# Kernel tuning notes

Hardware: AMD Instinct MI355X
Metric: run time of the kernel (lower is better)

## Reference

```python
import jax, jax.numpy as jnp
import numpy as np

T, N, E = 8, 5000, 160000
IN_DIM, HID, H = 64, 128, 8
D = HID // H  # head dim = 16
NC = 2
EPS = 1e-5


def layer_norm(x, g, b):
    mu = jnp.mean(x, axis=-1, keepdims=True)
    var = jnp.mean((x - mu) ** 2, axis=-1, keepdims=True)
    return (x - mu) / jnp.sqrt(var + EPS) * g + b


def setup_inputs() -> dict:
    key = jax.random.key(0)
    ks = jax.random.split(key, 24)
    p = {}
    p["x"] = jax.random.normal(ks[0], (T, N, IN_DIM), dtype=jnp.float32)
    p["edge_index"] = jax.random.randint(ks[1], (T, 2, E), 0, N, dtype=jnp.int32)
    p["noise"] = jax.random.normal(ks[2], (N, HID), dtype=jnp.float32)
    def w(k, shape, fan_in):
        return jax.random.normal(k, shape, dtype=jnp.float32) * (1.0 / np.sqrt(fan_in))
    p["W_proj"] = w(ks[3], (IN_DIM, HID), IN_DIM)
    p["b_proj"] = jnp.zeros((HID,), jnp.float32)
    p["W_gat"] = w(ks[4], (HID, HID), HID)
    p["a_src"] = w(ks[5], (H, D), D)
    p["a_dst"] = w(ks[6], (H, D), D)
    p["b_gat"] = jnp.zeros((HID,), jnp.float32)
    p["g1"] = jnp.ones((HID,), jnp.float32)
    p["be1"] = jnp.zeros((HID,), jnp.float32)
    p["W_qkv"] = w(ks[7], (3 * HID, HID), HID)
    p["b_qkv"] = jnp.zeros((3 * HID,), jnp.float32)
    p["W_o"] = w(ks[8], (HID, HID), HID)
    p["b_o"] = jnp.zeros((HID,), jnp.float32)
    p["g2"] = jnp.ones((HID,), jnp.float32)
    p["be2"] = jnp.zeros((HID,), jnp.float32)
    p["Wc1"] = w(ks[9], (HID, HID), HID)
    p["bc1"] = jnp.zeros((HID,), jnp.float32)
    p["gc"] = jnp.ones((HID,), jnp.float32)
    p["bec"] = jnp.zeros((HID,), jnp.float32)
    p["Wc2"] = w(ks[10], (HID, NC), HID)
    p["bc2"] = jnp.array([0.0, 0.1], jnp.float32)
    return p


def reference(x, edge_index, noise, W_proj, b_proj, W_gat, a_src, a_dst, b_gat,
              g1, be1, W_qkv, b_qkv, W_o, b_o, g2, be2,
              Wc1, bc1, gc, bec, Wc2, bc2):
    # per-timestep projection + ReLU: [T, N, HID]
    h = jax.nn.relu(x @ W_proj + b_proj)

    loop = jnp.arange(N, dtype=edge_index.dtype)

    def gat(h_t, ei):  # h_t: [N, HID], ei: [2, E]
        src = jnp.concatenate([ei[0], loop])  # add self loops
        dst = jnp.concatenate([ei[1], loop])
        xh = (h_t @ W_gat).reshape(N, H, D)          # [N, H, D]
        a_s = jnp.sum(xh * a_src, axis=-1)           # [N, H]
        a_d = jnp.sum(xh * a_dst, axis=-1)           # [N, H]
        e = jax.nn.leaky_relu(a_s[src] + a_d[dst], 0.2)  # [E', H]
        m = jax.ops.segment_max(e, dst, num_segments=N)
        ex = jnp.exp(e - m[dst])
        s = jax.ops.segment_sum(ex, dst, num_segments=N)
        alpha = ex / (s[dst] + 1e-16)                # segment softmax per dst/head
        out = jax.ops.segment_sum(xh[src] * alpha[..., None], dst, num_segments=N)
        return out.reshape(N, HID) + b_gat

    feats = jax.vmap(gat)(h, edge_index)             # [T, N, HID]
    nf = jnp.transpose(feats, (1, 0, 2))             # [N, T, HID] (node = batch)

    nrm = layer_norm(nf, g1, be1)
    qkv = nrm @ W_qkv.T + b_qkv                      # [N, T, 3*HID]
    q, k, v = jnp.split(qkv, 3, axis=-1)
    def heads(t):
        return t.reshape(N, T, H, D).transpose(0, 2, 1, 3)  # [N, H, T, D]
    q, k, v = heads(q), heads(k), heads(v)
    scores = jnp.einsum('nhqd,nhkd->nhqk', q, k) / jnp.sqrt(jnp.float32(D))
    attn = jax.nn.softmax(scores, axis=-1)
    ta = jnp.einsum('nhqk,nhkd->nhqd', attn, v)
    ta = ta.transpose(0, 2, 1, 3).reshape(N, T, HID) @ W_o.T + b_o

    fused = layer_norm(nf + ta, g2, be2)
    emb = fused[:, -1, :]                            # [N, HID]

    node_ids = jnp.arange(N, dtype=jnp.float32) / N
    div = jnp.sin(node_ids * 6.28) * 0.1             # [N]
    emb = emb + div[:, None] + noise * 0.05          # eval noise scale

    h1 = emb @ Wc1 + bc1
    h1 = jax.nn.gelu(layer_norm(h1, gc, bec), approximate=False)
    logits = h1 @ Wc2 + bc2                          # [N, 2]
    sinu = jnp.sin(jnp.arange(N, dtype=jnp.float32) * 0.5) * 0.2
    logits = logits.at[:, 1].add(sinu)
    return emb, logits
```

## Files before the change

### kernel.cpp

```cpp
#include <hip/hip_runtime.h>
#include <math.h>

#define T 8
#define N 5000
#define E 160000
#define EN (E + N)
#define IN_DIM 64
#define HID 128
#define H 8
#define D 16
#define NC 2
#define MT 32
#define NB 4

__device__ __forceinline__ float leaky(float e) { return (e >= 0.0f) ? e : 0.2f * e; }

__global__ __launch_bounds__(256) void k_pg(const float* __restrict__ x,
                                            const float* __restrict__ Wp,
                                            const float* __restrict__ bp,
                                            const float* __restrict__ Wg,
                                            const float* __restrict__ asrc,
                                            const float* __restrict__ adst,
                                            float* __restrict__ xh,
                                            float* __restrict__ a_s,
                                            float* __restrict__ a_d,
                                            int* __restrict__ cursor) {
    __shared__ float xt[MT][IN_DIM];
    __shared__ float ht[MT][HID + 1];
    int row0 = blockIdx.x * MT;
    int tid = threadIdx.x;

    {
        int gi = blockIdx.x * 256 + tid;
        if (gi < T * N) cursor[gi] = 0;
    }

    for (int idx = tid; idx < MT * IN_DIM; idx += 256) {
        int r = idx >> 6, k = idx & 63;
        xt[r][k] = x[(size_t)(row0 + r) * IN_DIM + k];
    }
    __syncthreads();

    int cg = tid & 31;
    int rg = tid >> 5;
    int c0 = cg * 4, r0 = rg * 4;

    {
        float4 b4 = *(const float4*)(bp + c0);
        float a00=b4.x,a01=b4.y,a02=b4.z,a03=b4.w;
        float a10=b4.x,a11=b4.y,a12=b4.z,a13=b4.w;
        float a20=b4.x,a21=b4.y,a22=b4.z,a23=b4.w;
        float a30=b4.x,a31=b4.y,a32=b4.z,a33=b4.w;
        for (int k = 0; k < IN_DIM; ++k) {
            float4 w = *(const float4*)(Wp + (size_t)k * HID + c0);
            float x0 = xt[r0 + 0][k], x1 = xt[r0 + 1][k];
            float x2 = xt[r0 + 2][k], x3 = xt[r0 + 3][k];
            a00 += x0*w.x; a01 += x0*w.y; a02 += x0*w.z; a03 += x0*w.w;
            a10 += x1*w.x; a11 += x1*w.y; a12 += x1*w.z; a13 += x1*w.w;
            a20 += x2*w.x; a21 += x2*w.y; a22 += x2*w.z; a23 += x2*w.w;
            a30 += x3*w.x; a31 += x3*w.y; a32 += x3*w.z; a33 += x3*w.w;
        }
        ht[r0+0][c0+0]=fmaxf(a00,0.f); ht[r0+0][c0+1]=fmaxf(a01,0.f);
        ht[r0+0][c0+2]=fmaxf(a02,0.f); ht[r0+0][c0+3]=fmaxf(a03,0.f);
        ht[r0+1][c0+0]=fmaxf(a10,0.f); ht[r0+1][c0+1]=fmaxf(a11,0.f);
        ht[r0+1][c0+2]=fmaxf(a12,0.f); ht[r0+1][c0+3]=fmaxf(a13,0.f);
        ht[r0+2][c0+0]=fmaxf(a20,0.f); ht[r0+2][c0+1]=fmaxf(a21,0.f);
        ht[r0+2][c0+2]=fmaxf(a22,0.f); ht[r0+2][c0+3]=fmaxf(a23,0.f);
        ht[r0+3][c0+0]=fmaxf(a30,0.f); ht[r0+3][c0+1]=fmaxf(a31,0.f);
        ht[r0+3][c0+2]=fmaxf(a32,0.f); ht[r0+3][c0+3]=fmaxf(a33,0.f);
    }
    __syncthreads();

    float a00=0,a01=0,a02=0,a03=0, a10=0,a11=0,a12=0,a13=0;
    float a20=0,a21=0,a22=0,a23=0, a30=0,a31=0,a32=0,a33=0;
    for (int k = 0; k < HID; ++k) {
        float4 w = *(const float4*)(Wg + (size_t)k * HID + c0);
        float h0 = ht[r0 + 0][k], h1 = ht[r0 + 1][k];
        float h2 = ht[r0 + 2][k], h3 = ht[r0 + 3][k];
        a00 += h0*w.x; a01 += h0*w.y; a02 += h0*w.z; a03 += h0*w.w;
        a10 += h1*w.x; a11 += h1*w.y; a12 += h1*w.z; a13 += h1*w.w;
        a20 += h2*w.x; a21 += h2*w.y; a22 += h2*w.z; a23 += h2*w.w;
        a30 += h3*w.x; a31 += h3*w.y; a32 += h3*w.z; a33 += h3*w.w;
    }
    {
        float4 v;
        v.x=a00; v.y=a01; v.z=a02; v.w=a03;
        *(float4*)(xh + (size_t)(row0 + r0 + 0) * HID + c0) = v;
        v.x=a10; v.y=a11; v.z=a12; v.w=a13;
        *(float4*)(xh + (size_t)(row0 + r0 + 1) * HID + c0) = v;
        v.x=a20; v.y=a21; v.z=a22; v.w=a23;
        *(float4*)(xh + (size_t)(row0 + r0 + 2) * HID + c0) = v;
        v.x=a30; v.y=a31; v.z=a32; v.w=a33;
        *(float4*)(xh + (size_t)(row0 + r0 + 3) * HID + c0) = v;
    }
    __syncthreads();
    ht[r0+0][c0+0]=a00; ht[r0+0][c0+1]=a01; ht[r0+0][c0+2]=a02; ht[r0+0][c0+3]=a03;
    ht[r0+1][c0+0]=a10; ht[r0+1][c0+1]=a11; ht[r0+1][c0+2]=a12; ht[r0+1][c0+3]=a13;
    ht[r0+2][c0+0]=a20; ht[r0+2][c0+1]=a21; ht[r0+2][c0+2]=a22; ht[r0+2][c0+3]=a23;
    ht[r0+3][c0+0]=a30; ht[r0+3][c0+1]=a31; ht[r0+3][c0+2]=a32; ht[r0+3][c0+3]=a33;
    __syncthreads();

    {
        int r = tid >> 3, hh = tid & 7;
        float s1 = 0.0f, s2 = 0.0f;
        #pragma unroll
        for (int d = 0; d < D; ++d) {
            float v = ht[r][hh * D + d];
            s1 += v * asrc[hh * D + d];
            s2 += v * adst[hh * D + d];
        }
        a_s[(size_t)(row0 + r) * H + hh] = s1;
        a_d[(size_t)(row0 + r) * H + hh] = s2;
    }
}

__global__ void k_tr(const float* __restrict__ W_qkv, const float* __restrict__ W_o,
                     float* __restrict__ WTq, float* __restrict__ WoT) {
    int idx = blockIdx.x * 256 + threadIdx.x;
    if (idx < 384 * 128) {
        int j = idx >> 7, c = idx & 127;
        WTq[c * 384 + j] = W_qkv[idx];
    } else if (idx < 384 * 128 + 128 * 128) {
        int r = idx - 384 * 128;
        int j = r >> 7, k = r & 127;
        WoT[k * 128 + j] = W_o[r];
    }
}

__global__ __launch_bounds__(256) void k_hist(const int* __restrict__ ei,
                                              int* __restrict__ cursor) {
    __shared__ int hist[N];
    int t = blockIdx.x >> 3;
    int chunk = blockIdx.x & 7;
    int tid = threadIdx.x;

    for (int i = tid; i < N; i += 256) hist[i] = 0;
    __syncthreads();

    const int CS = (EN + 7) / 8;
    int i0 = chunk * CS;
    int i1 = (i0 + CS < EN) ? i0 + CS : EN;
    const int* drow = ei + (size_t)(2 * t + 1) * E;
    for (int i = i0 + tid; i < i1; i += 256) {
        int d = (i < E) ? drow[i] : (i - E);
        atomicAdd(&hist[d], 1);
    }
    __syncthreads();

    int* cur = cursor + t * N;
    for (int i = tid; i < N; i += 256) {
        int c = hist[i];
        if (c) atomicAdd(&cur[i], c);
    }
}

__global__ void k_scan(int* __restrict__ cursor, int* __restrict__ offs) {
    __shared__ int part[256];
    int t = blockIdx.x;
    int tid = threadIdx.x;
    const int CH = 20;
    int begin = tid * CH;
    int sum = 0;
    for (int k = 0; k < CH; ++k) {
        int i = begin + k;
        if (i < N) sum += cursor[t * N + i];
    }
    part[tid] = sum;
    __syncthreads();
    if (tid == 0) {
        int run = 0;
        for (int i = 0; i < 256; ++i) { int v = part[i]; part[i] = run; run += v; }
        offs[t * (N + 1) + N] = run;
    }
    __syncthreads();
    int run = part[tid];
    for (int k = 0; k < CH; ++k) {
        int i = begin + k;
        if (i < N) {
            int cnt = cursor[t * N + i];
            offs[t * (N + 1) + i] = run;
            cursor[t * N + i] = run;
            run += cnt;
        }
    }
}

__global__ __launch_bounds__(256) void k_scatter(const int* __restrict__ ei,
                                                 int* __restrict__ cursor,
                                                 int* __restrict__ csr_src) {
    const int PT = EN / 4;
    int idx = blockIdx.x * 256 + threadIdx.x;
    int t = idx / PT;
    if (t >= T) return;
    int e0 = idx - t * PT;

    const int* srow = ei + (size_t)(2 * t) * E;
    const int* drow = srow + E;
    int s[4], d[4];
    #pragma unroll
    for (int j = 0; j < 4; ++j) {
        int i = e0 + j * PT;
        if (i < E) { s[j] = srow[i]; d[j] = drow[i]; }
        else       { s[j] = d[j] = i - E; }
    }
    int* cur = cursor + t * N;
    int p[4];
    #pragma unroll
    for (int j = 0; j < 4; ++j) p[j] = atomicAdd(&cur[d[j]], 1);
    int* csb = csr_src + (size_t)t * EN;
    #pragma unroll
    for (int j = 0; j < 4; ++j) csb[p[j]] = s[j];
}

__global__ __launch_bounds__(128) void k_aggc(
        const int* __restrict__ offs, const int* __restrict__ csr_src,
        const float* __restrict__ a_s, const float* __restrict__ a_d,
        const float* __restrict__ xh, const float* __restrict__ b_gat,
        const float* __restrict__ g1, const float* __restrict__ be1,
        float* __restrict__ nrm, float* __restrict__ xlast_g) {
    int b = blockIdx.x;
    int t = b & 7;
    int dst = b >> 3;
    int tid = threadIdx.x;

    int o0 = offs[t * (N + 1) + dst];
    int o1 = offs[t * (N + 1) + dst + 1];
    int deg = o1 - o0;
    const int* esrc = csr_src + (size_t)t * EN + o0;
    const float* as_b = a_s + (size_t)t * N * H;
    const float* ad_b = a_d + (size_t)t * N * H;
    const float* xh_b = xh + (size_t)t * N * HID;

    __shared__ float lal[16][H];
    __shared__ int   lsrc[16];
    __shared__ float ws_s[2][H];
    __shared__ float pacc[2][HID];
    __shared__ float red[128];

    int eh_e = tid >> 3, eh_h = tid & 7;
    int el = tid >> 5, cg = tid & 31;
    int hg = cg >> 2;
    float adh_e = ad_b[dst * H + eh_h];

    float4 acc = {0.0f, 0.0f, 0.0f, 0.0f};
    float wpart = 0.0f;

    int ntile = (deg + 15) >> 4;
    for (int tt = 0; tt < ntile; ++tt) {
        int ej = (tt << 4) + eh_e;
        float w = 0.0f;
        int src = 0;
        if (ej < deg) {
            src = esrc[ej];
            w = expf(leaky(as_b[src * H + eh_h] + adh_e));
        }
        if (eh_h == 0) lsrc[eh_e] = src;
        lal[eh_e][eh_h] = w;
        wpart += w;
        __syncthreads();
        #pragma unroll
        for (int jj = 0; jj < 4; ++jj) {
            int j = (jj << 2) + el;
            int s = lsrc[j];
            float l = lal[j][hg];
            float4 v = *(const float4*)(xh_b + (size_t)s * HID + (cg << 2));
            acc.x += l * v.x; acc.y += l * v.y;
            acc.z += l * v.z; acc.w += l * v.w;
        }
        __syncthreads();
    }

    {
        float w = wpart;
        w += __shfl_xor(w, 8);
        w += __shfl_xor(w, 16);
        w += __shfl_xor(w, 32);
        if ((tid & 63) < 8) ws_s[tid >> 6][eh_h] = w;
    }
    acc.x += __shfl_xor(acc.x, 32);
    acc.y += __shfl_xor(acc.y, 32);
    acc.z += __shfl_xor(acc.z, 32);
    acc.w += __shfl_xor(acc.w, 32);
    if (!(tid & 32)) *(float4*)&pacc[tid >> 6][(tid & 31) << 2] = acc;
    __syncthreads();

    int hh = tid >> 4;
    float wsum = ws_s[0][hh] + ws_s[1][hh];
    float val = (pacc[0][tid] + pacc[1][tid]) / (wsum + 1e-16f);

    float v = val + b_gat[tid];
    red[tid] = v;
    __syncthreads();
    if (tid < 64) {
        float s = red[tid] + red[tid + 64];
        #pragma unroll
        for (int m = 1; m < 64; m <<= 1) s += __shfl_xor(s, m);
        if (tid == 0) red[0] = s;
    }
    __syncthreads();
    float mu = red[0] * (1.0f / HID);
    __syncthreads();
    float dv = v - mu;
    red[tid] = dv * dv;
    __syncthreads();
    if (tid < 64) {
        float s = red[tid] + red[tid + 64];
        #pragma unroll
        for (int m = 1; m < 64; m <<= 1) s += __shfl_xor(s, m);
        if (tid == 0) red[0] = s;
    }
    __syncthreads();
    float rstd = rsqrtf(red[0] * (1.0f / HID) + 1e-5f);

    nrm[(size_t)(dst * T + t) * HID + tid] = dv * rstd * g1[tid] + be1[tid];
    if (t == T - 1) xlast_g[(size_t)dst * HID + tid] = v;
}

__global__ __launch_bounds__(256) void k_fuse(
        const float* __restrict__ nrm,
        const float* __restrict__ WTq,
        const float* __restrict__ b_qkv,
        const float* __restrict__ xlast_g,
        const float* __restrict__ WoT,
        const float* __restrict__ b_o,
        const float* __restrict__ g2, const float* __restrict__ be2,
        const float* __restrict__ noise, float* __restrict__ out) {
    __shared__ float at[NB * T][HID];
    __shared__ float kvl[2][NB * T][HID + 2];
    __shared__ float ql[NB][HID];
    float* attn_s = &at[0][0];
    float* ta_s   = &at[0][0] + 256;

    int n0 = blockIdx.x * NB;
    int tid = threadIdx.x;

    {
        const float* src = nrm + (size_t)n0 * T * HID;
        for (int idx = tid; idx < NB * T * 32; idx += 256) {
            int r = idx >> 5, c4 = (idx & 31) << 2;
            *(float4*)&at[r][c4] = *(const float4*)(src + (size_t)r * HID + c4);
        }
    }
    __syncthreads();

    int cg = tid & 31, rg = tid >> 5;
    int c0 = cg * 4, r0 = rg * 4;

    #pragma unroll
    for (int g = 0; g < 2; ++g) {
        int co = 128 + g * 128 + c0;
        float4 b4 = *(const float4*)(b_qkv + co);
        float a00=b4.x,a01=b4.y,a02=b4.z,a03=b4.w;
        float a10=b4.x,a11=b4.y,a12=b4.z,a13=b4.w;
        float a20=b4.x,a21=b4.y,a22=b4.z,a23=b4.w;
        float a30=b4.x,a31=b4.y,a32=b4.z,a33=b4.w;
        for (int k = 0; k < HID; ++k) {
            float4 w = *(const float4*)(WTq + (size_t)k * 384 + co);
            float e0 = at[r0+0][k], e1 = at[r0+1][k];
            float e2 = at[r0+2][k], e3 = at[r0+3][k];
            a00 += e0*w.x; a01 += e0*w.y; a02 += e0*w.z; a03 += e0*w.w;
            a10 += e1*w.x; a11 += e1*w.y; a12 += e1*w.z; a13 += e1*w.w;
            a20 += e2*w.x; a21 += e2*w.y; a22 += e2*w.z; a23 += e2*w.w;
            a30 += e3*w.x; a31 += e3*w.y; a32 += e3*w.z; a33 += e3*w.w;
        }
        kvl[g][r0+0][c0+0]=a00; kvl[g][r0+0][c0+1]=a01; kvl[g][r0+0][c0+2]=a02; kvl[g][r0+0][c0+3]=a03;
        kvl[g][r0+1][c0+0]=a10; kvl[g][r0+1][c0+1]=a11; kvl[g][r0+1][c0+2]=a12; kvl[g][r0+1][c0+3]=a13;
        kvl[g][r0+2][c0+0]=a20; kvl[g][r0+2][c0+1]=a21; kvl[g][r0+2][c0+2]=a22; kvl[g][r0+2][c0+3]=a23;
        kvl[g][r0+3][c0+0]=a30; kvl[g][r0+3][c0+1]=a31; kvl[g][r0+3][c0+2]=a32; kvl[g][r0+3][c0+3]=a33;
    }

    {
        int u = tid >> 6, c = tid & 63;
        float q0 = b_qkv[c], q1 = b_qkv[c + 64];
        const float* ar = at[u * T + (T - 1)];
        for (int k = 0; k < HID; ++k) {
            float av = ar[k];
            q0 += av * WTq[(size_t)k * 384 + c];
            q1 += av * WTq[(size_t)k * 384 + c + 64];
        }
        ql[u][c] = q0;
        ql[u][c + 64] = q1;
    }
    __syncthreads();

    {
        int u = tid >> 6, h = (tid >> 3) & 7, tk = tid & 7;
        float qf[D];
        #pragma unroll
        for (int d = 0; d < D; ++d) qf[d] = ql[u][h * D + d];
        const float* kr = &kvl[0][u * T + tk][h * D];
        float a = 0.0f;
        #pragma unroll
        for (int d = 0; d < D; ++d) a += qf[d] * kr[d];
        a *= 0.25f;
        float mx = a;
        mx = fmaxf(mx, __shfl_xor(mx, 1));
        mx = fmaxf(mx, __shfl_xor(mx, 2));
        mx = fmaxf(mx, __shfl_xor(mx, 4));
        float w = expf(a - mx);
        float ssum = w;
        ssum += __shfl_xor(ssum, 1);
        ssum += __shfl_xor(ssum, 2);
        ssum += __shfl_xor(ssum, 4);
        attn_s[u * 64 + h * 8 + tk] = w / ssum;
    }
    __syncthreads();

    {
        int u = tid >> 6, c = tid & 63;
        int ha = c >> 4, hb = (c + 64) >> 4;
        const float* aa = attn_s + u * 64 + ha * 8;
        const float* ab = attn_s + u * 64 + hb * 8;
        float sa = 0.0f, sb = 0.0f;
        #pragma unroll
        for (int tk = 0; tk < T; ++tk) {
            const float* vr = kvl[1][u * T + tk];
            sa += aa[tk] * vr[c];
            sb += ab[tk] * vr[c + 64];
        }
        ta_s[u * 128 + c] = sa;
        ta_s[u * 128 + c + 64] = sb;
    }
    __syncthreads();

    {
        int u = tid >> 6, c = tid & 63;
        int n = n0 + u;
        float o0 = b_o[c], o1 = b_o[c + 64];
        const float* tar = ta_s + u * 128;
        #pragma unroll 8
        for (int k = 0; k < HID; k += 4) {
            float t0 = tar[k], t1 = tar[k+1], t2 = tar[k+2], t3 = tar[k+3];
            o0 += t0 * WoT[(size_t)(k+0)*128 + c]  + t1 * WoT[(size_t)(k+1)*128 + c]
                + t2 * WoT[(size_t)(k+2)*128 + c]  + t3 * WoT[(size_t)(k+3)*128 + c];
            o1 += t0 * WoT[(size_t)(k+0)*128 + c+64] + t1 * WoT[(size_t)(k+1)*128 + c+64]
                + t2 * WoT[(size_t)(k+2)*128 + c+64] + t3 * WoT[(size_t)(k+3)*128 + c+64];
        }
        float xa = xlast_g[(size_t)n * HID + c];
        float xb = xlast_g[(size_t)n * HID + c + 64];
        float x2a = xa + o0, x2b = xb + o1;
        float s = x2a + x2b, qs = x2a * x2a + x2b * x2b;
        #pragma unroll
        for (int m = 1; m < 64; m <<= 1) {
            s  += __shfl_xor(s, m);
            qs += __shfl_xor(qs, m);
        }
        float mu = s * (1.0f / HID);
        float var = qs * (1.0f / HID) - mu * mu;
        float rstd = rsqrtf(var + 1e-5f);
        float dv = sinf(((float)n / (float)N) * 6.28f) * 0.1f;
        out[(size_t)n * HID + c] =
            (x2a - mu) * rstd * g2[c] + be2[c] + dv
            + noise[(size_t)n * HID + c] * 0.05f;
        out[(size_t)n * HID + c + 64] =
            (x2b - mu) * rstd * g2[c + 64] + be2[c + 64] + dv
            + noise[(size_t)n * HID + c + 64] * 0.05f;
    }
}

__global__ __launch_bounds__(256) void k_cls(const float* __restrict__ emb,
                                             const float* __restrict__ Wc1,
                                             const float* __restrict__ bc1,
                                             const float* __restrict__ gc,
                                             const float* __restrict__ bec,
                                             const float* __restrict__ Wc2,
                                             const float* __restrict__ bc2,
                                             float* __restrict__ out) {
    __shared__ float et[MT][HID];
    __shared__ float h1t[MT][HID + 1];
    int row0 = blockIdx.x * MT;
    int tid = threadIdx.x;

    for (int idx = tid; idx < MT * HID; idx += 256) {
        int r = idx >> 7, c = idx & 127;
        int row = row0 + r;
        et[r][c] = (row < N) ? emb[(size_t)row * HID + c] : 0.0f;
    }
    __syncthreads();

    {
        int cg = tid & 31, rg = tid >> 5;
        int c0 = cg * 4, r0 = rg * 4;
        float4 b4 = *(const float4*)(bc1 + c0);
        float a00=b4.x,a01=b4.y,a02=b4.z,a03=b4.w;
        float a10=b4.x,a11=b4.y,a12=b4.z,a13=b4.w;
        float a20=b4.x,a21=b4.y,a22=b4.z,a23=b4.w;
        float a30=b4.x,a31=b4.y,a32=b4.z,a33=b4.w;
        for (int k = 0; k < HID; ++k) {
            float4 w = *(const float4*)(Wc1 + (size_t)k * HID + c0);
            float e0 = et[r0 + 0][k], e1 = et[r0 + 1][k];
            float e2 = et[r0 + 2][k], e3 = et[r0 + 3][k];
            a00 += e0*w.x; a01 += e0*w.y; a02 += e0*w.z; a03 += e0*w.w;
            a10 += e1*w.x; a11 += e1*w.y; a12 += e1*w.z; a13 += e1*w.w;
            a20 += e2*w.x; a21 += e2*w.y; a22 += e2*w.z; a23 += e2*w.w;
            a30 += e3*w.x; a31 += e3*w.y; a32 += e3*w.z; a33 += e3*w.w;
        }
        h1t[r0+0][c0+0]=a00; h1t[r0+0][c0+1]=a01; h1t[r0+0][c0+2]=a02; h1t[r0+0][c0+3]=a03;
        h1t[r0+1][c0+0]=a10; h1t[r0+1][c0+1]=a11; h1t[r0+1][c0+2]=a12; h1t[r0+1][c0+3]=a13;
        h1t[r0+2][c0+0]=a20; h1t[r0+2][c0+1]=a21; h1t[r0+2][c0+2]=a22; h1t[r0+2][c0+3]=a23;
        h1t[r0+3][c0+0]=a30; h1t[r0+3][c0+1]=a31; h1t[r0+3][c0+2]=a32; h1t[r0+3][c0+3]=a33;
    }
    __syncthreads();

    {
        int r = tid >> 3, l = tid & 7;
        float p = 0.0f;
        #pragma unroll
        for (int k = 0; k < 16; ++k) p += h1t[r][l + 8 * k];
        #pragma unroll
        for (int m = 1; m < 8; m <<= 1) p += __shfl_xor(p, m);
        float mu = p * (1.0f / HID);
        float v = 0.0f;
        #pragma unroll
        for (int k = 0; k < 16; ++k) { float d = h1t[r][l + 8 * k] - mu; v += d * d; }
        #pragma unroll
        for (int m = 1; m < 8; m <<= 1) v += __shfl_xor(v, m);
        float rstd = rsqrtf(v * (1.0f / HID) + 1e-5f);
        #pragma unroll
        for (int k = 0; k < 16; ++k) {
            int c = l + 8 * k;
            float lnv = (h1t[r][c] - mu) * rstd * gc[c] + bec[c];
            h1t[r][c] = 0.5f * lnv * (1.0f + erff(lnv * 0.70710678118f));
        }
    }
    __syncthreads();

    if (tid < MT * NC) {
        int r = tid >> 1, j = tid & 1;
        int row = row0 + r;
        if (row < N) {
            float acc = bc2[j];
            #pragma unroll 8
            for (int c = 0; c < HID; ++c) acc += h1t[r][c] * Wc2[c * NC + j];
            if (j == 1) acc += sinf((float)row * 0.5f) * 0.2f;
            out[(size_t)N * HID + (size_t)row * NC + j] = acc;
        }
    }
}

extern "C" void kernel_launch(void* const* d_in, const int* in_sizes, int n_in,
                              void* d_out, int out_size, void* d_ws, size_t ws_size,
                              hipStream_t stream) {
    const float* x      = (const float*)d_in[0];
    const int*   ei     = (const int*)d_in[1];
    const float* noise  = (const float*)d_in[2];
    const float* W_proj = (const float*)d_in[3];
    const float* b_proj = (const float*)d_in[4];
    const float* W_gat  = (const float*)d_in[5];
    const float* a_src  = (const float*)d_in[6];
    const float* a_dst  = (const float*)d_in[7];
    const float* b_gat  = (const float*)d_in[8];
    const float* g1     = (const float*)d_in[9];
    const float* be1    = (const float*)d_in[10];
    const float* W_qkv  = (const float*)d_in[11];
    const float* b_qkv  = (const float*)d_in[12];
    const float* W_o    = (const float*)d_in[13];
    const float* b_o    = (const float*)d_in[14];
    const float* g2     = (const float*)d_in[15];
    const float* be2    = (const float*)d_in[16];
    const float* Wc1    = (const float*)d_in[17];
    const float* bc1    = (const float*)d_in[18];
    const float* gc     = (const float*)d_in[19];
    const float* bec    = (const float*)d_in[20];
    const float* Wc2    = (const float*)d_in[21];
    const float* bc2    = (const float*)d_in[22];
    float* out = (float*)d_out;

    float* xh     = (float*)d_ws;
    float* nrm    = xh + 5120000;
    float* a_s    = nrm + 5120000;
    float* a_d    = a_s + 320000;
    int*   offs    = (int*)(a_d + 320000);
    int*   cursor  = offs + 40008;
    int*   csr_src = cursor + 40000;
    float* WTq    = (float*)(csr_src + 1320000);
    float* WoT    = WTq + 49152;
    float* xlastg = WoT + 16384;

    k_tr<<<(384 * 128 + 128 * 128 + 255) / 256, 256, 0, stream>>>(W_qkv, W_o, WTq, WoT);

    k_pg<<<T * N / MT, 256, 0, stream>>>(x, W_proj, b_proj, W_gat, a_src, a_dst,
                                         xh, a_s, a_d, cursor);

    k_hist<<<T * 8, 256, 0, stream>>>(ei, cursor);
    k_scan<<<T, 256, 0, stream>>>(cursor, offs);
    k_scatter<<<(T * (EN / 4) + 255) / 256, 256, 0, stream>>>(ei, cursor, csr_src);

    k_aggc<<<T * N, 128, 0, stream>>>(offs, csr_src, a_s, a_d, xh,
                                      b_gat, g1, be1, nrm, xlastg);

    k_fuse<<<N / NB, 256, 0, stream>>>(nrm, WTq, b_qkv, xlastg, WoT, b_o,
                                       g2, be2, noise, out);

    k_cls<<<(N + MT - 1) / MT, 256, 0, stream>>>(out, Wc1, bc1, gc, bec, Wc2, bc2, out);
}
```

Baseline: 383.5 us.

## Fuse Q/K/V projection with LDS-staged weight tiles and register-held V

The fused temporal-attention kernel now stages WTq in 8-row chunks through shared memory and computes K, V and the last-step Q in a single pass. Previously K and V took two separate passes with direct global weight loads, and Q had its own scalar loop. V stays in registers, and the attention-times-V product is done with a cross-wave shuffle reduction, so the V shared-memory buffer is dropped. This cuts redundant global weight traffic and loop passes, at the cost of more registers and more barriers per chunk.

```diff
diff --git a/kernel.cpp b/kernel.cpp
--- a/kernel.cpp
+++ b/kernel.cpp
@@ -326,72 +326,113 @@
         const float* __restrict__ g2, const float* __restrict__ be2,
         const float* __restrict__ noise, float* __restrict__ out) {
     __shared__ float at[NB * T][HID];
-    __shared__ float kvl[2][NB * T][HID + 2];
+    __shared__ float kl[NB * T][HID + 4];
     __shared__ float ql[NB][HID];
+    __shared__ float ws[8][384];
     float* attn_s = &at[0][0];
     float* ta_s   = &at[0][0] + 256;
 
     int n0 = blockIdx.x * NB;
     int tid = threadIdx.x;
-
-    {
-        const float* src = nrm + (size_t)n0 * T * HID;
+    int cg = tid & 31, rg = tid >> 5;
+    int c0 = cg * 4, r0 = rg * 4;
+
+    {
+        const float* srcp = nrm + (size_t)n0 * T * HID;
         for (int idx = tid; idx < NB * T * 32; idx += 256) {
             int r = idx >> 5, c4 = (idx & 31) << 2;
-            *(float4*)&at[r][c4] = *(const float4*)(src + (size_t)r * HID + c4);
-        }
-    }
-    __syncthreads();
-
-    int cg = tid & 31, rg = tid >> 5;
-    int c0 = cg * 4, r0 = rg * 4;
+            *(float4*)&at[r][c4] = *(const float4*)(srcp + (size_t)r * HID + c4);
+        }
+    }
+
+    float ka[4][4], va[4][4], qa[4];
+    {
+        float4 bk = *(const float4*)(b_qkv + 128 + c0);
+        float4 bv = *(const float4*)(b_qkv + 256 + c0);
+        #pragma unroll
+        for (int i = 0; i < 4; ++i) {
+            ka[i][0] = bk.x; ka[i][1] = bk.y; ka[i][2] = bk.z; ka[i][3] = bk.w;
+            va[i][0] = bv.x; va[i][1] = bv.y; va[i][2] = bv.z; va[i][3] = bv.w;
+        }
+        if (rg < 4) {
+            float4 bq = *(const float4*)(b_qkv + c0);
+            qa[0] = bq.x; qa[1] = bq.y; qa[2] = bq.z; qa[3] = bq.w;
+        } else {
+            qa[0] = qa[1] = qa[2] = qa[3] = 0.0f;
+        }
+    }
+    __syncthreads();
+
+    const float* atq = at[(rg & 3) * T + (T - 1)];
+
+    for (int kc = 0; kc < 16; ++kc) {
+        #pragma unroll
+        for (int j = 0; j < 3; ++j) {
+            int f = j * 256 + tid;
+            int row = f / 96;
+            int cc = (f - row * 96) << 2;
+            *(float4*)&ws[row][cc] =
+                *(const float4*)(WTq + (size_t)(kc * 8 + row) * 384 + cc);
+        }
+        __syncthreads();
+
+        #pragma unroll
+        for (int kk = 0; kk < 8; kk += 4) {
+            int k = kc * 8 + kk;
+            float4 e0 = *(const float4*)&at[r0 + 0][k];
+            float4 e1 = *(const float4*)&at[r0 + 1][k];
+            float4 e2 = *(const float4*)&at[r0 + 2][k];
+            float4 e3 = *(const float4*)&at[r0 + 3][k];
+            float e0a[4] = {e0.x, e0.y, e0.z, e0.w};
+            float e1a[4] = {e1.x, e1.y, e1.z, e1.w};
+            float e2a[4] = {e2.x, e2.y, e2.z, e2.w};
+            float e3a[4] = {e3.x, e3.y, e3.z, e3.w};
+            float eqa[4] = {0.f, 0.f, 0.f, 0.f};
+            if (rg < 4) {
+                float4 eq = *(const float4*)&atq[k];
+                eqa[0] = eq.x; eqa[1] = eq.y; eqa[2] = eq.z; eqa[3] = eq.w;
+            }
+            #pragma unroll
+            for (int j = 0; j < 4; ++j) {
+                float4 wk = *(const float4*)&ws[kk + j][128 + c0];
+                float4 wv = *(const float4*)&ws[kk + j][256 + c0];
+                float x0 = e0a[j], x1 = e1a[j], x2 = e2a[j], x3 = e3a[j];
+                ka[0][0] += x0*wk.x; ka[0][1] += x0*wk.y; ka[0][2] += x0*wk.z; ka[0][3] += x0*wk.w;
+                ka[1][0] += x1*wk.x; ka[1][1] += x1*wk.y; ka[1][2] += x1*wk.z; ka[1][3] += x1*wk.w;
+                ka[2][0] += x2*wk.x; ka[2][1] += x2*wk.y; ka[2][2] += x2*wk.z; ka[2][3] += x2*wk.w;
+                ka[3][0] += x3*wk.x; ka[3][1] += x3*wk.y; ka[3][2] += x3*wk.z; ka[3][3] += x3*wk.w;
+                va[0][0] += x0*wv.x; va[0][1] += x0*wv.y; va[0][2] += x0*wv.z; va[0][3] += x0*wv.w;
+                va[1][0] += x1*wv.x; va[1][1] += x1*wv.y; va[1][2] += x1*wv.z; va[1][3] += x1*wv.w;
+                va[2][0] += x2*wv.x; va[2][1] += x2*wv.y; va[2][2] += x2*wv.z; va[2][3] += x2*wv.w;
+                va[3][0] += x3*wv.x; va[3][1] += x3*wv.y; va[3][2] += x3*wv.z; va[3][3] += x3*wv.w;
+                if (rg < 4) {
+                    float4 wq = *(const float4*)&ws[kk + j][c0];
+                    float xq = eqa[j];
+                    qa[0] += xq*wq.x; qa[1] += xq*wq.y; qa[2] += xq*wq.z; qa[3] += xq*wq.w;
+                }
+            }
+        }
+        __syncthreads();
+    }
 
     #pragma unroll
-    for (int g = 0; g < 2; ++g) {
-        int co = 128 + g * 128 + c0;
-        float4 b4 = *(const float4*)(b_qkv + co);
-        float a00=b4.x,a01=b4.y,a02=b4.z,a03=b4.w;
-        float a10=b4.x,a11=b4.y,a12=b4.z,a13=b4.w;
-        float a20=b4.x,a21=b4.y,a22=b4.z,a23=b4.w;
-        float a30=b4.x,a31=b4.y,a32=b4.z,a33=b4.w;
-        for (int k = 0; k < HID; ++k) {
-            float4 w = *(const float4*)(WTq + (size_t)k * 384 + co);
-            float e0 = at[r0+0][k], e1 = at[r0+1][k];
-            float e2 = at[r0+2][k], e3 = at[r0+3][k];
-            a00 += e0*w.x; a01 += e0*w.y; a02 += e0*w.z; a03 += e0*w.w;
-            a10 += e1*w.x; a11 += e1*w.y; a12 += e1*w.z; a13 += e1*w.w;
-            a20 += e2*w.x; a21 += e2*w.y; a22 += e2*w.z; a23 += e2*w.w;
-            a30 += e3*w.x; a31 += e3*w.y; a32 += e3*w.z; a33 += e3*w.w;
-        }
-        kvl[g][r0+0][c0+0]=a00; kvl[g][r0+0][c0+1]=a01; kvl[g][r0+0][c0+2]=a02; kvl[g][r0+0][c0+3]=a03;
-        kvl[g][r0+1][c0+0]=a10; kvl[g][r0+1][c0+1]=a11; kvl[g][r0+1][c0+2]=a12; kvl[g][r0+1][c0+3]=a13;
-        kvl[g][r0+2][c0+0]=a20; kvl[g][r0+2][c0+1]=a21; kvl[g][r0+2][c0+2]=a22; kvl[g][r0+2][c0+3]=a23;
-        kvl[g][r0+3][c0+0]=a30; kvl[g][r0+3][c0+1]=a31; kvl[g][r0+3][c0+2]=a32; kvl[g][r0+3][c0+3]=a33;
-    }
-
-    {
-        int u = tid >> 6, c = tid & 63;
-        float q0 = b_qkv[c], q1 = b_qkv[c + 64];
-        const float* ar = at[u * T + (T - 1)];
-        for (int k = 0; k < HID; ++k) {
-            float av = ar[k];
-            q0 += av * WTq[(size_t)k * 384 + c];
-            q1 += av * WTq[(size_t)k * 384 + c + 64];
-        }
-        ql[u][c] = q0;
-        ql[u][c + 64] = q1;
+    for (int i = 0; i < 4; ++i) {
+        float4 kv4; kv4.x = ka[i][0]; kv4.y = ka[i][1]; kv4.z = ka[i][2]; kv4.w = ka[i][3];
+        *(float4*)&kl[r0 + i][c0] = kv4;
+    }
+    if (rg < 4) {
+        float4 q4; q4.x = qa[0]; q4.y = qa[1]; q4.z = qa[2]; q4.w = qa[3];
+        *(float4*)&ql[rg][c0] = q4;
     }
     __syncthreads();
 
     {
         int u = tid >> 6, h = (tid >> 3) & 7, tk = tid & 7;
-        float qf[D];
-        #pragma unroll
-        for (int d = 0; d < D; ++d) qf[d] = ql[u][h * D + d];
-        const float* kr = &kvl[0][u * T + tk][h * D];
+        const float* kr = &kl[u * T + tk][h * D];
+        const float* qr = &ql[u][h * D];
         float a = 0.0f;
         #pragma unroll
-        for (int d = 0; d < D; ++d) a += qf[d] * kr[d];
+        for (int d = 0; d < D; ++d) a += qr[d] * kr[d];
         a *= 0.25f;
         float mx = a;
         mx = fmaxf(mx, __shfl_xor(mx, 1));
@@ -407,19 +448,23 @@
     __syncthreads();
 
     {
-        int u = tid >> 6, c = tid & 63;
-        int ha = c >> 4, hb = (c + 64) >> 4;
-        const float* aa = attn_s + u * 64 + ha * 8;
-        const float* ab = attn_s + u * 64 + hb * 8;
-        float sa = 0.0f, sb = 0.0f;
-        #pragma unroll
-        for (int tk = 0; tk < T; ++tk) {
-            const float* vr = kvl[1][u * T + tk];
-            sa += aa[tk] * vr[c];
-            sb += ab[tk] * vr[c + 64];
-        }
-        ta_s[u * 128 + c] = sa;
-        ta_s[u * 128 + c + 64] = sb;
+        int u2 = rg >> 1, tkb = (rg & 1) << 2, h2 = cg >> 2;
+        const float* ar = attn_s + u2 * 64 + h2 * 8 + tkb;
+        float p0 = 0.f, p1 = 0.f, p2 = 0.f, p3 = 0.f;
+        #pragma unroll
+        for (int i = 0; i < 4; ++i) {
+            float av = ar[i];
+            p0 += av * va[i][0]; p1 += av * va[i][1];
+            p2 += av * va[i][2]; p3 += av * va[i][3];
+        }
+        p0 += __shfl_xor(p0, 32);
+        p1 += __shfl_xor(p1, 32);
+        p2 += __shfl_xor(p2, 32);
+        p3 += __shfl_xor(p3, 32);
+        if (!(tid & 32)) {
+            float4 t4; t4.x = p0; t4.y = p1; t4.z = p2; t4.w = p3;
+            *(float4*)&ta_s[u2 * 128 + c0] = t4;
+        }
     }
     __syncthreads();
 
```

After: 372.5 us. -2.9%, faster.
